# Kernel tuning notes

Measured on AMD Instinct MI355X. Metric: run time of the kernel, lower is better.

## Reference

```python
import jax, jax.numpy as jnp
import numpy as np

NUM_USERS = 50000
NUM_ITEMS = 50000
N_NODES = NUM_USERS + NUM_ITEMS
NNZ = 3200000
EMB_DIM = 64
N_LAYERS = 3
BATCH = 16384


def setup_inputs() -> dict:
    key = jax.random.key(0)
    ks = jax.random.split(key, 7)
    user_emb = 0.1 * jax.random.normal(ks[0], (NUM_USERS, EMB_DIM), dtype=jnp.float32)
    item_emb = 0.1 * jax.random.normal(ks[1], (NUM_ITEMS, EMB_DIM), dtype=jnp.float32)
    edge_val = jax.random.uniform(ks[2], (NNZ,), dtype=jnp.float32)
    edge_src = jax.random.randint(ks[3], (NNZ,), 0, N_NODES, dtype=jnp.int32)
    edge_dst = jax.random.randint(ks[4], (NNZ,), 0, N_NODES, dtype=jnp.int32)
    users = jax.random.randint(ks[5], (BATCH,), 0, NUM_USERS, dtype=jnp.int32)
    items = jax.random.randint(ks[6], (BATCH,), 0, NUM_ITEMS, dtype=jnp.int32)
    return {"user_emb": user_emb, "item_emb": item_emb, "edge_val": edge_val,
            "edge_src": edge_src, "edge_dst": edge_dst, "users": users, "items": items}


def _computer(user_emb, item_emb, edge_val, edge_src, edge_dst):
    # LightGCN propagation: all_emb <- A @ all_emb, mean over layer outputs (incl. layer 0)
    all_emb = jnp.concatenate([user_emb, item_emb], axis=0)  # [N, D]
    acc = all_emb
    for _ in range(N_LAYERS):
        msg = edge_val[:, None] * all_emb[edge_src]          # [nnz, D]
        all_emb = jax.ops.segment_sum(msg, edge_dst, num_segments=N_NODES)
        acc = acc + all_emb
    light_out = acc / jnp.float32(N_LAYERS + 1)
    return light_out[:NUM_USERS], light_out[NUM_USERS:]


def reference(user_emb, item_emb, edge_val, edge_src, edge_dst, users, items):
    all_users, all_items = _computer(user_emb, item_emb, edge_val, edge_src, edge_dst)
    users_emb = all_users[users]                              # [B, D]
    items_emb = all_items[items]                              # [B, D]
    gamma = jnp.sum(users_emb * items_emb, axis=1)            # [B]
    return gamma
```

## Files before the change

### kernel.cpp

```cpp
#include <hip/hip_runtime.h>

#define NUM_USERS 50000
#define NUM_ITEMS 50000
#define N_NODES   100000
#define NNZ       3200000
#define EMB_DIM   64
#define N_LAYERS  3
#define BATCH     16384

#define NBUCK 512
#define ABITS 8
#define NODES_PER_BUCK 256
#define TILE_EDGES 8192
#define NBUCK_USED ((N_NODES + NODES_PER_BUCK - 1) / NODES_PER_BUCK)
#define CAP 9472
#define NCELL 1024

typedef unsigned long long ull;
typedef float v2f __attribute__((ext_vector_type(2)));
typedef unsigned v4u __attribute__((ext_vector_type(4)));

__device__ inline unsigned bf16pair(float a, float b) {
    unsigned ua = __float_as_uint(a), ub = __float_as_uint(b);
    unsigned r0 = (ua + 0x7fffu + ((ua >> 16) & 1u)) >> 16;
    unsigned r1 = (ub + 0x7fffu + ((ub >> 16) & 1u)) >> 16;
    return r0 | (r1 << 16);
}
__device__ inline float blo(unsigned u) { return __uint_as_float(u << 16); }
__device__ inline float bhi(unsigned u) { return __uint_as_float(u & 0xffff0000u); }

__device__ inline void pkfma(v2f& d, v2f a, v2f b) {
    asm("v_pk_fma_f32 %0, %1, %2, %0" : "+v"(d) : "v"(a), "v"(b));
}
__device__ inline void pkadd(v2f& d, v2f a) {
    asm("v_pk_add_f32 %0, %1, %0" : "+v"(d) : "v"(a));
}

__device__ inline void accP(v2f& sA, v2f& sB, v2f& sC, v2f& sD, uint4 g, unsigned r) {
    float w = (float)(r >> 17);
    v2f w2 = {w, w};
    v2f e0 = {blo(g.x), bhi(g.x)};
    v2f e1 = {blo(g.y), bhi(g.y)};
    v2f e2 = {blo(g.z), bhi(g.z)};
    v2f e3 = {blo(g.w), bhi(g.w)};
    pkfma(sA, e0, w2);
    pkfma(sB, e1, w2);
    pkfma(sC, e2, w2);
    pkfma(sD, e3, w2);
}

__device__ inline uint4 gath(const unsigned char* __restrict__ base, unsigned r, unsigned dOff) {
    unsigned off = ((r & 0x1FFFFu) << 7) + dOff;
    return *(const uint4*)(base + off);
}

__device__ inline unsigned ntl(const unsigned* __restrict__ p) {
    return __builtin_nontemporal_load(p);
}

__device__ inline void wred(v2f& s) {
    v2f t;
    t.x = __shfl_xor(s.x, 8, 64);  t.y = __shfl_xor(s.y, 8, 64);  pkadd(s, t);
    t.x = __shfl_xor(s.x, 16, 64); t.y = __shfl_xor(s.y, 16, 64); pkadd(s, t);
    t.x = __shfl_xor(s.x, 32, 64); t.y = __shfl_xor(s.y, 32, 64); pkadd(s, t);
}

__device__ inline void pull_node(const unsigned char* __restrict__ A16,
                                 unsigned* __restrict__ B16,
                                 const unsigned* __restrict__ sorted,
                                 int node, int start, int cnt, int lane) {
    int eg = lane >> 3;
    int d8 = lane & 7;
    unsigned dOff = (unsigned)d8 << 4;
    const unsigned* ep = sorted + start;

    v2f sA = {0.f,0.f}, sB = {0.f,0.f}, sC = {0.f,0.f}, sD = {0.f,0.f};
    int j = 0;
    while (j + 32 <= cnt) {
        unsigned r0 = ntl(ep + j + eg),      r1 = ntl(ep + j + 8 + eg);
        unsigned r2 = ntl(ep + j + 16 + eg), r3 = ntl(ep + j + 24 + eg);
        uint4 g0 = gath(A16, r0, dOff);
        uint4 g1 = gath(A16, r1, dOff);
        uint4 g2 = gath(A16, r2, dOff);
        uint4 g3 = gath(A16, r3, dOff);
        accP(sA, sB, sC, sD, g0, r0);
        accP(sA, sB, sC, sD, g1, r1);
        accP(sA, sB, sC, sD, g2, r2);
        accP(sA, sB, sC, sD, g3, r3);
        j += 32;
    }
    if (j + 16 <= cnt) {
        unsigned r0 = ntl(ep + j + eg), r1 = ntl(ep + j + 8 + eg);
        uint4 g0 = gath(A16, r0, dOff);
        uint4 g1 = gath(A16, r1, dOff);
        accP(sA, sB, sC, sD, g0, r0);
        accP(sA, sB, sC, sD, g1, r1);
        j += 16;
    }
    if (j < cnt) {
        int i0 = j + eg, i1 = j + 8 + eg;
        unsigned r0 = (i0 < cnt) ? ntl(ep + i0) : 0u;
        unsigned r1 = (i1 < cnt) ? ntl(ep + i1) : 0u;
        uint4 g0 = gath(A16, r0, dOff);
        uint4 g1 = gath(A16, r1, dOff);
        accP(sA, sB, sC, sD, g0, r0);
        accP(sA, sB, sC, sD, g1, r1);
    }

    wred(sA); wred(sB); wred(sC); wred(sD);

    if (eg == 0) {
        const float k15 = 1.f / 32768.f;
        v4u h;
        h.x = bf16pair(sA.x * k15, sA.y * k15);
        h.y = bf16pair(sB.x * k15, sB.y * k15);
        h.z = bf16pair(sC.x * k15, sC.y * k15);
        h.w = bf16pair(sD.x * k15, sD.y * k15);
        v4u* dst = (v4u*)(B16 + (((long long)node) << 5) + ((long long)d8 << 2));
        __builtin_nontemporal_store(h, dst);
    }
}

__global__ void init_emb_kernel(const float* __restrict__ ue,
                                const float* __restrict__ ie,
                                unsigned* __restrict__ E0,
                                int* __restrict__ bucketCursor) {
    int idx = blockIdx.x * blockDim.x + threadIdx.x;
    if (blockIdx.x == 0 && threadIdx.x < 256) {
        bucketCursor[threadIdx.x]       = threadIdx.x * CAP;
        bucketCursor[threadIdx.x + 256] = (threadIdx.x + 256) * CAP;
    }
    const int total = N_NODES * (EMB_DIM / 4);
    if (idx >= total) return;
    const int uoff = NUM_USERS * (EMB_DIM / 4);
    float4 v;
    if (idx < uoff) v = ((const float4*)ue)[idx];
    else            v = ((const float4*)ie)[idx - uoff];
    uint2 h;
    h.x = bf16pair(v.x, v.y);
    h.y = bf16pair(v.z, v.w);
    ((uint2*)E0)[idx] = h;
}

__global__ void partA_kernel(const float* __restrict__ ev,
                             const int*  __restrict__ es,
                             const int*  __restrict__ ed,
                             int* __restrict__ bucketCursor,
                             ull* __restrict__ tmp) {
    __shared__ int hist[NBUCK];
    __shared__ int base[NBUCK];
    __shared__ int cnt2[NBUCK];
    int tid = threadIdx.x;
    int e0 = blockIdx.x * TILE_EDGES;

    int      mySrc[8], myDst[8];
    unsigned myQ[8];

    for (int i = tid; i < NBUCK; i += 1024) hist[i] = 0;
    __syncthreads();

    #pragma unroll
    for (int k = 0; k < 8; ++k) {
        int e = e0 + k * 1024 + tid;
        if (e < NNZ) {
            mySrc[k] = es[e];
            myDst[k] = ed[e];
            myQ[k]   = (unsigned)fminf(ev[e] * 32768.f + 0.5f, 32767.f);
            atomicAdd(&hist[((unsigned)myDst[k]) >> ABITS], 1);
        } else {
            myDst[k] = -1;
        }
    }
    __syncthreads();

    for (int i = tid; i < NBUCK; i += 1024) {
        int c = hist[i];
        base[i] = c ? atomicAdd(&bucketCursor[i], c) : 0;
        cnt2[i] = 0;
    }
    __syncthreads();

    #pragma unroll
    for (int k = 0; k < 8; ++k) {
        int dst = myDst[k];
        if (dst < 0) continue;
        int b = ((unsigned)dst) >> ABITS;
        int pos = base[b] + atomicAdd(&cnt2[b], 1);
        if (pos < (b + 1) * CAP) {
            ull rec = (ull)(unsigned)(mySrc[k] | ((dst & (NODES_PER_BUCK - 1)) << 17))
                    | ((ull)myQ[k] << 25);
            tmp[pos] = rec;
        }
    }
}

__global__ void partB_kernel(const ull* __restrict__ tmp,
                             const int* __restrict__ bucketCursor,
                             int* __restrict__ rowStart,
                             int* __restrict__ deg,
                             unsigned* __restrict__ sorted) {
    __shared__ int cnt[NCELL];
    __shared__ int nsc[NODES_PER_BUCK];
    __shared__ int nstart[NODES_PER_BUCK];
    __shared__ int cur[NCELL];
    int b = blockIdx.x;
    int tid = threadIdx.x;
    int nodeLo = b << ABITS;
    int startE = b * CAP;
    int endE   = bucketCursor[b];

    cnt[tid] = 0;
    __syncthreads();

    ull myRec[9];
    int myCell[9];
    int nRec = 0;
    #pragma unroll
    for (int k = 0; k < 9; ++k) {
        int i = startE + k * 1024 + tid;
        if (i < endE) {
            myRec[k] = tmp[i];
            nRec = k + 1;
            unsigned src = (unsigned)(myRec[k] & 0x1FFFFULL);
            int q = (int)(src >> 15); if (q > 3) q = 3;
            int dl = (int)((myRec[k] >> 17) & (NODES_PER_BUCK - 1));
            myCell[k] = (dl << 2) + q;
            atomicAdd(&cnt[myCell[k]], 1);
        }
    }
    __syncthreads();

    int p4 = 0;
    if (tid < NODES_PER_BUCK) {
        int tot = cnt[tid*4] + cnt[tid*4+1] + cnt[tid*4+2] + cnt[tid*4+3];
        p4 = (tot + 3) & ~3;
        nsc[tid] = p4;
    }
    __syncthreads();
    for (int o = 1; o < NODES_PER_BUCK; o <<= 1) {
        int add = 0;
        if (tid < NODES_PER_BUCK && tid >= o) add = nsc[tid - o];
        __syncthreads();
        if (tid < NODES_PER_BUCK) nsc[tid] += add;
        __syncthreads();
    }
    if (tid < NODES_PER_BUCK) {
        int ns = startE + nsc[tid] - p4;
        nstart[tid] = ns;
        int node = nodeLo + tid;
        if (node < N_NODES) {
            rowStart[node] = ns;
            deg[node] = p4;
        }
    }
    __syncthreads();

    {
        int n = tid >> 2, q = tid & 3;
        int c = nstart[n];
        if (q > 0) c += cnt[n*4];
        if (q > 1) c += cnt[n*4+1];
        if (q > 2) c += cnt[n*4+2];
        cur[tid] = c;
    }
    __syncthreads();

    for (int k = 0; k < nRec; ++k) {
        ull rec = myRec[k];
        unsigned o = (unsigned)(rec & 0x1FFFFULL) | ((unsigned)((rec >> 25) & 0x7FFF) << 17);
        int pos = atomicAdd(&cur[myCell[k]], 1);
        if (pos < startE + CAP) sorted[pos] = o;
    }
    __syncthreads();

    if (tid < NODES_PER_BUCK) {
        int tot = cnt[tid*4] + cnt[tid*4+1] + cnt[tid*4+2] + cnt[tid*4+3];
        int end = nstart[tid] + ((tot + 3) & ~3);
        for (int p = nstart[tid] + tot; p < end; ++p)
            if (p < startE + CAP) sorted[p] = 0;
    }
}

__global__ void pull_sync_kernel(const unsigned char* __restrict__ A16,
                                 unsigned* __restrict__ B16,
                                 const unsigned* __restrict__ sorted,
                                 const int* __restrict__ rowStart,
                                 const int* __restrict__ deg) {
    int t = blockIdx.x * blockDim.x + threadIdx.x;
    int node = __builtin_amdgcn_readfirstlane(t >> 6);
    if (node >= N_NODES) return;
    int start = rowStart[node];
    int cnt   = deg[node];
    pull_node(A16, B16, sorted, node, start, cnt, t & 63);
}

__global__ void pull_gated_kernel(const unsigned char* __restrict__ A16,
                                  unsigned* __restrict__ B16,
                                  const unsigned* __restrict__ sorted,
                                  const int* __restrict__ rowStart,
                                  const int* __restrict__ deg,
                                  const int* __restrict__ users,
                                  const int* __restrict__ items) {
    int t = blockIdx.x * blockDim.x + threadIdx.x;
    int e = __builtin_amdgcn_readfirstlane(t >> 6);
    if (e >= 2 * BATCH) return;
    int node = (e < BATCH) ? users[e] : (NUM_USERS + items[e - BATCH]);
    node = __builtin_amdgcn_readfirstlane(node);
    int start = rowStart[node];
    int cnt   = deg[node];
    pull_node(A16, B16, sorted, node, start, cnt, t & 63);
}

__global__ void dot_kernel(const unsigned* __restrict__ E0,
                           const unsigned* __restrict__ B1,
                           const unsigned* __restrict__ B2,
                           const unsigned* __restrict__ B3,
                           const int* __restrict__ users,
                           const int* __restrict__ items,
                           float* __restrict__ out) {
    int t = blockIdx.x * blockDim.x + threadIdx.x;
    int b = t >> 5;
    int lane = t & 31;
    if (b >= BATCH) return;
    long long uo = ((long long)users[b] << 5) + lane;
    long long io = ((long long)(items[b] + NUM_USERS) << 5) + lane;
    unsigned a0 = E0[uo], a1 = B1[uo], a2 = B2[uo], a3 = B3[uo];
    unsigned c0 = E0[io], c1 = B1[io], c2 = B2[io], c3 = B3[io];
    float ux = (blo(a0) + blo(a1)) + (blo(a2) + blo(a3));
    float uy = (bhi(a0) + bhi(a1)) + (bhi(a2) + bhi(a3));
    float ix = (blo(c0) + blo(c1)) + (blo(c2) + blo(c3));
    float iy = (bhi(c0) + bhi(c1)) + (bhi(c2) + bhi(c3));
    float p = ux * ix + uy * iy;
    #pragma unroll
    for (int off = 16; off >= 1; off >>= 1)
        p += __shfl_xor(p, off, 64);
    if (lane == 0) out[b] = p * 0.0625f;
}

extern "C" void kernel_launch(void* const* d_in, const int* in_sizes, int n_in,
                              void* d_out, int out_size, void* d_ws, size_t ws_size,
                              hipStream_t stream) {
    const float* user_emb = (const float*)d_in[0];
    const float* item_emb = (const float*)d_in[1];
    const float* edge_val = (const float*)d_in[2];
    const int*   edge_src = (const int*)d_in[3];
    const int*   edge_dst = (const int*)d_in[4];
    const int*   users    = (const int*)d_in[5];
    const int*   items    = (const int*)d_in[6];
    float* out = (float*)d_out;

    const size_t emb16Bytes = (size_t)N_NODES * EMB_DIM * 2;
    const size_t sortBytes  = (size_t)NBUCK_USED * CAP * sizeof(unsigned);
    const size_t tmpBytes   = (size_t)NBUCK_USED * CAP * sizeof(ull);
    const size_t nodeBytes  = (size_t)N_NODES * sizeof(int);

    char* w = (char*)d_ws;
    unsigned* E0           = (unsigned*)(w); w += emb16Bytes;
    unsigned* B1           = (unsigned*)(w); w += emb16Bytes;
    unsigned* B2           = (unsigned*)(w); w += emb16Bytes;
    unsigned* B3           = (unsigned*)(w); w += emb16Bytes;
    unsigned* sorted       = (unsigned*)(w); w += sortBytes;
    ull*      tmp          = (ull*)(w);      w += tmpBytes;
    int*      deg          = (int*)(w);      w += nodeBytes;
    int*      rowStart     = (int*)(w);      w += nodeBytes;
    int*      bucketCursor = (int*)(w);      w += NBUCK * sizeof(int);

    const int vecTotal   = N_NODES * (EMB_DIM / 4);
    const int initBlocks = (vecTotal + 255) / 256;
    const int tileBlocks = (NNZ + TILE_EDGES - 1) / TILE_EDGES;

    init_emb_kernel<<<initBlocks, 256, 0, stream>>>(user_emb, item_emb, E0, bucketCursor);

    partA_kernel<<<tileBlocks, 1024, 0, stream>>>(edge_val, edge_src, edge_dst,
                                                  bucketCursor, tmp);
    partB_kernel<<<NBUCK_USED, 1024, 0, stream>>>(tmp, bucketCursor,
                                                  rowStart, deg, sorted);

    const int pullBlocks = (N_NODES * 64 + 255) / 256;
    pull_sync_kernel<<<pullBlocks, 256, 0, stream>>>((const unsigned char*)E0, B1,
                                                     sorted, rowStart, deg);
    pull_sync_kernel<<<pullBlocks, 256, 0, stream>>>((const unsigned char*)B1, B2,
                                                     sorted, rowStart, deg);

    const int gatedBlocks = (2 * BATCH * 64 + 255) / 256;
    pull_gated_kernel<<<gatedBlocks, 256, 0, stream>>>((const unsigned char*)B2, B3,
                                                       sorted, rowStart, deg, users, items);

    const int dotBlocks = (BATCH * 32 + 255) / 256;
    dot_kernel<<<dotBlocks, 256, 0, stream>>>(E0, B1, B2, B3, users, items, out);
}
```

Before: 279.5 us.

## Split partition records into 4B+1B streams, drop src sub-binning, vectorize edge loads

The temporary partition buffer moves from packed 8-byte records to a 4-byte record array (src|weight) plus a 1-byte local-destination array, which cuts the traffic between partA and partB. partB no longer sub-sorts each node's edges into four source-range cells, so it needs less shared memory and fewer steps, at the possible cost of gather locality in the pull kernels. The pull loop now reads four edge records per lane with one 16-byte load instead of four strided nontemporal loads, and the output store becomes a normal store. Changing the per-lane edge assignment is safe because the lanes are summed by the wave reduction.

```diff
diff --git a/kernel.cpp b/kernel.cpp
--- a/kernel.cpp
+++ b/kernel.cpp
@@ -14,11 +14,9 @@
 #define TILE_EDGES 8192
 #define NBUCK_USED ((N_NODES + NODES_PER_BUCK - 1) / NODES_PER_BUCK)
 #define CAP 9472
-#define NCELL 1024
 
 typedef unsigned long long ull;
 typedef float v2f __attribute__((ext_vector_type(2)));
-typedef unsigned v4u __attribute__((ext_vector_type(4)));
 
 __device__ inline unsigned bf16pair(float a, float b) {
     unsigned ua = __float_as_uint(a), ub = __float_as_uint(b);
@@ -54,10 +52,6 @@
     return *(const uint4*)(base + off);
 }
 
-__device__ inline unsigned ntl(const unsigned* __restrict__ p) {
-    return __builtin_nontemporal_load(p);
-}
-
 __device__ inline void wred(v2f& s) {
     v2f t;
     t.x = __shfl_xor(s.x, 8, 64);  t.y = __shfl_xor(s.y, 8, 64);  pkadd(s, t);
@@ -77,47 +71,46 @@
     v2f sA = {0.f,0.f}, sB = {0.f,0.f}, sC = {0.f,0.f}, sD = {0.f,0.f};
     int j = 0;
     while (j + 32 <= cnt) {
-        unsigned r0 = ntl(ep + j + eg),      r1 = ntl(ep + j + 8 + eg);
-        unsigned r2 = ntl(ep + j + 16 + eg), r3 = ntl(ep + j + 24 + eg);
-        uint4 g0 = gath(A16, r0, dOff);
-        uint4 g1 = gath(A16, r1, dOff);
-        uint4 g2 = gath(A16, r2, dOff);
-        uint4 g3 = gath(A16, r3, dOff);
-        accP(sA, sB, sC, sD, g0, r0);
-        accP(sA, sB, sC, sD, g1, r1);
-        accP(sA, sB, sC, sD, g2, r2);
-        accP(sA, sB, sC, sD, g3, r3);
+        uint4 R = *(const uint4*)(ep + j + (eg << 2));
+        uint4 g0 = gath(A16, R.x, dOff);
+        uint4 g1 = gath(A16, R.y, dOff);
+        uint4 g2 = gath(A16, R.z, dOff);
+        uint4 g3 = gath(A16, R.w, dOff);
+        accP(sA, sB, sC, sD, g0, R.x);
+        accP(sA, sB, sC, sD, g1, R.y);
+        accP(sA, sB, sC, sD, g2, R.z);
+        accP(sA, sB, sC, sD, g3, R.w);
         j += 32;
     }
-    if (j + 16 <= cnt) {
-        unsigned r0 = ntl(ep + j + eg), r1 = ntl(ep + j + 8 + eg);
+    int rem = cnt - j;
+    if (rem >= 16) {
+        uint2 R = *(const uint2*)(ep + j + (eg << 1));
+        uint4 g0 = gath(A16, R.x, dOff);
+        uint4 g1 = gath(A16, R.y, dOff);
+        accP(sA, sB, sC, sD, g0, R.x);
+        accP(sA, sB, sC, sD, g1, R.y);
+        j += 16; rem -= 16;
+    }
+    if (rem > 0) {
+        int i0 = j + eg, i1 = j + 8 + eg;
+        unsigned r0 = (i0 < cnt) ? ep[i0] : 0u;
+        unsigned r1 = (i1 < cnt) ? ep[i1] : 0u;
         uint4 g0 = gath(A16, r0, dOff);
         uint4 g1 = gath(A16, r1, dOff);
         accP(sA, sB, sC, sD, g0, r0);
         accP(sA, sB, sC, sD, g1, r1);
-        j += 16;
-    }
-    if (j < cnt) {
-        int i0 = j + eg, i1 = j + 8 + eg;
-        unsigned r0 = (i0 < cnt) ? ntl(ep + i0) : 0u;
-        unsigned r1 = (i1 < cnt) ? ntl(ep + i1) : 0u;
-        uint4 g0 = gath(A16, r0, dOff);
-        uint4 g1 = gath(A16, r1, dOff);
-        accP(sA, sB, sC, sD, g0, r0);
-        accP(sA, sB, sC, sD, g1, r1);
     }
 
     wred(sA); wred(sB); wred(sC); wred(sD);
 
     if (eg == 0) {
         const float k15 = 1.f / 32768.f;
-        v4u h;
+        uint4 h;
         h.x = bf16pair(sA.x * k15, sA.y * k15);
         h.y = bf16pair(sB.x * k15, sB.y * k15);
         h.z = bf16pair(sC.x * k15, sC.y * k15);
         h.w = bf16pair(sD.x * k15, sD.y * k15);
-        v4u* dst = (v4u*)(B16 + (((long long)node) << 5) + ((long long)d8 << 2));
-        __builtin_nontemporal_store(h, dst);
+        *(uint4*)(B16 + (((long long)node) << 5) + (d8 << 2)) = h;
     }
 }
 
@@ -146,15 +139,16 @@
                              const int*  __restrict__ es,
                              const int*  __restrict__ ed,
                              int* __restrict__ bucketCursor,
-                             ull* __restrict__ tmp) {
+                             unsigned* __restrict__ tmpR,
+                             unsigned char* __restrict__ tmpD) {
     __shared__ int hist[NBUCK];
     __shared__ int base[NBUCK];
     __shared__ int cnt2[NBUCK];
     int tid = threadIdx.x;
     int e0 = blockIdx.x * TILE_EDGES;
 
-    int      mySrc[8], myDst[8];
-    unsigned myQ[8];
+    int      myDst[8];
+    unsigned myR[8];
 
     for (int i = tid; i < NBUCK; i += 1024) hist[i] = 0;
     __syncthreads();
@@ -163,9 +157,9 @@
     for (int k = 0; k < 8; ++k) {
         int e = e0 + k * 1024 + tid;
         if (e < NNZ) {
-            mySrc[k] = es[e];
             myDst[k] = ed[e];
-            myQ[k]   = (unsigned)fminf(ev[e] * 32768.f + 0.5f, 32767.f);
+            unsigned q = (unsigned)fminf(ev[e] * 32768.f + 0.5f, 32767.f);
+            myR[k] = (unsigned)es[e] | (q << 17);
             atomicAdd(&hist[((unsigned)myDst[k]) >> ABITS], 1);
         } else {
             myDst[k] = -1;
@@ -187,53 +181,49 @@
         int b = ((unsigned)dst) >> ABITS;
         int pos = base[b] + atomicAdd(&cnt2[b], 1);
         if (pos < (b + 1) * CAP) {
-            ull rec = (ull)(unsigned)(mySrc[k] | ((dst & (NODES_PER_BUCK - 1)) << 17))
-                    | ((ull)myQ[k] << 25);
-            tmp[pos] = rec;
+            tmpR[pos] = myR[k];
+            tmpD[pos] = (unsigned char)(dst & (NODES_PER_BUCK - 1));
         }
     }
 }
 
-__global__ void partB_kernel(const ull* __restrict__ tmp,
+__global__ void partB_kernel(const unsigned* __restrict__ tmpR,
+                             const unsigned char* __restrict__ tmpD,
                              const int* __restrict__ bucketCursor,
                              int* __restrict__ rowStart,
                              int* __restrict__ deg,
                              unsigned* __restrict__ sorted) {
-    __shared__ int cnt[NCELL];
+    __shared__ int cnt[NODES_PER_BUCK];
     __shared__ int nsc[NODES_PER_BUCK];
     __shared__ int nstart[NODES_PER_BUCK];
-    __shared__ int cur[NCELL];
+    __shared__ int cur[NODES_PER_BUCK];
     int b = blockIdx.x;
     int tid = threadIdx.x;
     int nodeLo = b << ABITS;
     int startE = b * CAP;
     int endE   = bucketCursor[b];
 
-    cnt[tid] = 0;
-    __syncthreads();
-
-    ull myRec[9];
-    int myCell[9];
+    if (tid < NODES_PER_BUCK) cnt[tid] = 0;
+    __syncthreads();
+
+    unsigned myRec[9];
+    int myDl[9];
     int nRec = 0;
     #pragma unroll
     for (int k = 0; k < 9; ++k) {
         int i = startE + k * 1024 + tid;
         if (i < endE) {
-            myRec[k] = tmp[i];
+            myRec[k] = tmpR[i];
+            myDl[k]  = (int)tmpD[i];
             nRec = k + 1;
-            unsigned src = (unsigned)(myRec[k] & 0x1FFFFULL);
-            int q = (int)(src >> 15); if (q > 3) q = 3;
-            int dl = (int)((myRec[k] >> 17) & (NODES_PER_BUCK - 1));
-            myCell[k] = (dl << 2) + q;
-            atomicAdd(&cnt[myCell[k]], 1);
+            atomicAdd(&cnt[myDl[k]], 1);
         }
     }
     __syncthreads();
 
     int p4 = 0;
     if (tid < NODES_PER_BUCK) {
-        int tot = cnt[tid*4] + cnt[tid*4+1] + cnt[tid*4+2] + cnt[tid*4+3];
-        p4 = (tot + 3) & ~3;
+        p4 = (cnt[tid] + 3) & ~3;
         nsc[tid] = p4;
     }
     __syncthreads();
@@ -247,6 +237,7 @@
     if (tid < NODES_PER_BUCK) {
         int ns = startE + nsc[tid] - p4;
         nstart[tid] = ns;
+        cur[tid] = ns;
         int node = nodeLo + tid;
         if (node < N_NODES) {
             rowStart[node] = ns;
@@ -255,28 +246,15 @@
     }
     __syncthreads();
 
-    {
-        int n = tid >> 2, q = tid & 3;
-        int c = nstart[n];
-        if (q > 0) c += cnt[n*4];
-        if (q > 1) c += cnt[n*4+1];
-        if (q > 2) c += cnt[n*4+2];
-        cur[tid] = c;
-    }
-    __syncthreads();
-
     for (int k = 0; k < nRec; ++k) {
-        ull rec = myRec[k];
-        unsigned o = (unsigned)(rec & 0x1FFFFULL) | ((unsigned)((rec >> 25) & 0x7FFF) << 17);
-        int pos = atomicAdd(&cur[myCell[k]], 1);
-        if (pos < startE + CAP) sorted[pos] = o;
+        int pos = atomicAdd(&cur[myDl[k]], 1);
+        if (pos < startE + CAP) sorted[pos] = myRec[k];
     }
     __syncthreads();
 
     if (tid < NODES_PER_BUCK) {
-        int tot = cnt[tid*4] + cnt[tid*4+1] + cnt[tid*4+2] + cnt[tid*4+3];
-        int end = nstart[tid] + ((tot + 3) & ~3);
-        for (int p = nstart[tid] + tot; p < end; ++p)
+        int end = nstart[tid] + ((cnt[tid] + 3) & ~3);
+        for (int p = cur[tid]; p < end; ++p)
             if (p < startE + CAP) sorted[p] = 0;
     }
 }
@@ -351,7 +329,8 @@
 
     const size_t emb16Bytes = (size_t)N_NODES * EMB_DIM * 2;
     const size_t sortBytes  = (size_t)NBUCK_USED * CAP * sizeof(unsigned);
-    const size_t tmpBytes   = (size_t)NBUCK_USED * CAP * sizeof(ull);
+    const size_t tmpRBytes  = (size_t)NBUCK_USED * CAP * sizeof(unsigned);
+    const size_t tmpDBytes  = (size_t)NBUCK_USED * CAP;
     const size_t nodeBytes  = (size_t)N_NODES * sizeof(int);
 
     char* w = (char*)d_ws;
@@ -360,7 +339,8 @@
     unsigned* B2           = (unsigned*)(w); w += emb16Bytes;
     unsigned* B3           = (unsigned*)(w); w += emb16Bytes;
     unsigned* sorted       = (unsigned*)(w); w += sortBytes;
-    ull*      tmp          = (ull*)(w);      w += tmpBytes;
+    unsigned* tmpR         = (unsigned*)(w); w += tmpRBytes;
+    unsigned char* tmpD    = (unsigned char*)(w); w += (tmpDBytes + 15) & ~15ull;
     int*      deg          = (int*)(w);      w += nodeBytes;
     int*      rowStart     = (int*)(w);      w += nodeBytes;
     int*      bucketCursor = (int*)(w);      w += NBUCK * sizeof(int);
@@ -372,8 +352,8 @@
     init_emb_kernel<<<initBlocks, 256, 0, stream>>>(user_emb, item_emb, E0, bucketCursor);
 
     partA_kernel<<<tileBlocks, 1024, 0, stream>>>(edge_val, edge_src, edge_dst,
-                                                  bucketCursor, tmp);
-    partB_kernel<<<NBUCK_USED, 1024, 0, stream>>>(tmp, bucketCursor,
+                                                  bucketCursor, tmpR, tmpD);
+    partB_kernel<<<NBUCK_USED, 1024, 0, stream>>>(tmpR, tmpD, bucketCursor,
                                                   rowStart, deg, sorted);
 
     const int pullBlocks = (N_NODES * 64 + 255) / 256;
```

Measured after the change: 294.2 us. +5.2%, slower.
